# Kernel optimization log

Measured on AMD Instinct MI355X. Metric: run time of the kernel, lower is better.

Reference implementation:

```python
import jax, jax.numpy as jnp
import numpy as np

EPS = 1e-5

def _ln(x, g, b):
    m = x.mean(-1, keepdims=True)
    v = x.var(-1, keepdims=True)
    return (x - m) / jnp.sqrt(v + EPS) * g + b

def _dwconv(x, w, b, stride, pad):
    # x: [B,C,H,W], w: [C,1,k,k] depthwise
    C = x.shape[1]
    y = jax.lax.conv_general_dilated(
        x, w, (stride, stride), pad,
        feature_group_count=C,
        dimension_numbers=('NCHW', 'OIHW', 'NCHW'))
    return y + b[None, :, None, None]

def setup_inputs() -> dict:
    key = jax.random.key(0)
    ks = jax.random.split(key, 16)
    B, H, W, C = 8, 64, 64, 256
    N = H * W
    sr = 8
    d = {}
    d['x'] = jax.random.normal(ks[0], (B, N, C), jnp.float32)
    d['q_w'] = jax.random.normal(ks[1], (C, C), jnp.float32) * 0.02
    d['kv1_w'] = jax.random.normal(ks[2], (C, C), jnp.float32) * 0.02
    d['kv2_w'] = jax.random.normal(ks[3], (C, C), jnp.float32) * 0.02
    d['proj_w'] = jax.random.normal(ks[4], (C, C), jnp.float32) * 0.02
    d['proj_b'] = jnp.zeros((C,), jnp.float32)
    k1 = sr // 2
    d['sr1_w'] = jax.random.normal(ks[5], (C, 1, k1, k1), jnp.float32) * np.sqrt(2.0 / (k1 * k1))
    d['sr1_b'] = jnp.zeros((C,), jnp.float32)
    d['sr2_w'] = jax.random.normal(ks[6], (C, 1, sr, sr), jnp.float32) * np.sqrt(2.0 / (sr * sr))
    d['sr2_b'] = jnp.zeros((C,), jnp.float32)
    d['ln1_g'] = jnp.ones((C,), jnp.float32)
    d['ln1_b'] = jnp.zeros((C,), jnp.float32)
    d['ln2_g'] = jnp.ones((C,), jnp.float32)
    d['ln2_b'] = jnp.zeros((C,), jnp.float32)
    d['lc1_w'] = jax.random.normal(ks[7], (C // 2, 1, 3, 3), jnp.float32) * np.sqrt(2.0 / 9.0)
    d['lc1_b'] = jnp.zeros((C // 2,), jnp.float32)
    d['lc2_w'] = jax.random.normal(ks[8], (C // 2, 1, 3, 3), jnp.float32) * np.sqrt(2.0 / 9.0)
    d['lc2_b'] = jnp.zeros((C // 2,), jnp.float32)
    d['H'] = H
    d['W'] = W
    return d

def reference(x, q_w, kv1_w, kv2_w, proj_w, proj_b,
              sr1_w, sr1_b, sr2_w, sr2_b,
              ln1_g, ln1_b, ln2_g, ln2_b,
              lc1_w, lc1_b, lc2_w, lc2_b, H, W):
    B, N, C = x.shape
    nh = 8
    nh2 = nh // 2
    hd = C // nh
    sr = 8
    scale = hd ** -0.5

    # q: [B, nh, N, hd]
    q = jnp.einsum('bnc,dc->bnd', x, q_w).reshape(B, N, nh, hd).transpose(0, 2, 1, 3)

    x_ = x.transpose(0, 2, 1).reshape(B, C, H, W)
    x1 = _dwconv(x_, sr1_w, sr1_b, sr // 2, 'VALID')            # [B,C,H/4,W/4]
    x1 = x1.reshape(B, C, -1).transpose(0, 2, 1)                 # [B,N1,C]
    x1 = jax.nn.gelu(_ln(x1, ln1_g, ln1_b), approximate=False)
    x2 = _dwconv(x_, sr2_w, sr2_b, sr, 'VALID')                  # [B,C,H/8,W/8]
    x2 = x2.reshape(B, C, -1).transpose(0, 2, 1)                 # [B,N2,C]
    x2 = jax.nn.gelu(_ln(x2, ln2_g, ln2_b), approximate=False)

    def branch(xr, kv_w, qh, Hs, Ws, lc_w, lc_b):
        Bn, Ns, _ = xr.shape
        kv = jnp.einsum('bnc,dc->bnd', xr, kv_w).reshape(Bn, Ns, 2, nh2, hd).transpose(2, 0, 3, 1, 4)
        k, v = kv[0], kv[1]                                      # [B,nh2,Ns,hd]
        attn = jax.nn.softmax(jnp.einsum('bhqd,bhkd->bhqk', qh, k) * scale, axis=-1)
        # depthwise local conv injected into v
        v_sp = v.transpose(0, 2, 1, 3).reshape(Bn, Ns, C // 2).transpose(0, 2, 1).reshape(Bn, C // 2, Hs, Ws)
        v_lc = _dwconv(v_sp, lc_w, lc_b, 1, ((1, 1), (1, 1)))
        v = v + v_lc.reshape(Bn, nh2, hd, Ns).transpose(0, 1, 3, 2)
        out = jnp.einsum('bhqk,bhkd->bhqd', attn, v)             # [B,nh2,N,hd]
        return out.transpose(0, 2, 1, 3).reshape(Bn, N, C // 2)

    o1 = branch(x1, kv1_w, q[:, :nh2], H * 2 // sr, W * 2 // sr, lc1_w, lc1_b)
    o2 = branch(x2, kv2_w, q[:, nh2:], H // sr, W // sr, lc2_w, lc2_b)
    out = jnp.concatenate([o1, o2], axis=-1)
    return jnp.einsum('bnc,dc->bnd', out, proj_w) + proj_b
```

## Files before the change

### kernel.cpp

```cpp
#include <hip/hip_runtime.h>
#include <math.h>

static constexpr int Bb  = 8;
static constexpr int Nn  = 4096;
static constexpr int Cc  = 256;
static constexpr int Wd  = 64;
static constexpr int N1c = 256;
static constexpr int N2c = 64;

typedef __attribute__((ext_vector_type(8))) _Float16 f16x8;
typedef __attribute__((ext_vector_type(4))) _Float16 f16x4;
typedef __attribute__((ext_vector_type(4))) float    f32x4v;

__global__ __launch_bounds__(256)
void cvt4f16(const float* __restrict__ w0, const float* __restrict__ w1,
             const float* __restrict__ w2, const float* __restrict__ w3,
             _Float16* __restrict__ wf) {
  const int wsel = blockIdx.y;
  const float* w = wsel == 0 ? w0 : wsel == 1 ? w1 : wsel == 2 ? w2 : w3;
  const int i = (blockIdx.x * 256 + threadIdx.x) * 4;
  float4 v = *(const float4*)(w + i);
  f16x4 o = {(_Float16)v.x, (_Float16)v.y, (_Float16)v.z, (_Float16)v.w};
  *(f16x4*)(wf + (size_t)wsel * 65536 + i) = o;
}

template<bool A_HALF, bool OUT_HALF, bool BIAS>
__global__ __launch_bounds__(256)
void gemm_lds(const void* __restrict__ Ain, const _Float16* __restrict__ Wf,
              const float* __restrict__ bias, void* __restrict__ Outv) {
  __shared__ _Float16 Asl[2][64][40];
  __shared__ _Float16 Bsl[2][256][40];
  const int tid = threadIdx.x, lane = tid & 63, wid = tid >> 6;
  const int qi = lane & 15, g = lane >> 4;
  const int m0 = blockIdx.x * 64;
  const int ar = tid >> 2, ak = (tid & 3) * 8;

  const float*    pa32 = (const float*)Ain    + (size_t)(m0 + ar) * 256 + ak;
  const _Float16* pa16 = (const _Float16*)Ain + (size_t)(m0 + ar) * 256 + ak;
  const _Float16* pw   = Wf + (size_t)tid * 256;

  f32x4v acc[4][4] = {};
  f16x8 rA; f16x8 rB[4];

#define LDREG(k0)                                                        \
  do {                                                                   \
    if (A_HALF) {                                                        \
      rA = *(const f16x8*)(pa16 + (k0));                                 \
    } else {                                                             \
      float4 t0 = *(const float4*)(pa32 + (k0));                         \
      float4 t1 = *(const float4*)(pa32 + (k0) + 4);                     \
      rA = (f16x8){(_Float16)t0.x, (_Float16)t0.y, (_Float16)t0.z,       \
                   (_Float16)t0.w, (_Float16)t1.x, (_Float16)t1.y,       \
                   (_Float16)t1.z, (_Float16)t1.w};                      \
    }                                                                    \
    _Pragma("unroll")                                                    \
    for (int i = 0; i < 4; ++i) rB[i] = *(const f16x8*)(pw + (k0) + i * 8); \
  } while (0)

#define DSWRITE(buf)                                                     \
  do {                                                                   \
    *(f16x8*)&Asl[buf][ar][ak] = rA;                                     \
    _Pragma("unroll")                                                    \
    for (int i = 0; i < 4; ++i) *(f16x8*)&Bsl[buf][tid][i * 8] = rB[i];  \
  } while (0)

  LDREG(0);
  DSWRITE(0);
  LDREG(32);
  __syncthreads();

#pragma unroll
  for (int ks = 0; ks < 8; ++ks) {
    const int cur = ks & 1;
    if (ks < 7) DSWRITE(cur ^ 1);
    if (ks < 6) LDREG((ks + 2) * 32);
    f16x8 af[4], bf[4];
#pragma unroll
    for (int mt = 0; mt < 4; ++mt)
      af[mt] = *(const f16x8*)&Asl[cur][mt * 16 + qi][g * 8];
#pragma unroll
    for (int nt = 0; nt < 4; ++nt)
      bf[nt] = *(const f16x8*)&Bsl[cur][wid * 64 + nt * 16 + qi][g * 8];
#pragma unroll
    for (int nt = 0; nt < 4; ++nt)
#pragma unroll
      for (int mt = 0; mt < 4; ++mt)
        acc[mt][nt] = __builtin_amdgcn_mfma_f32_16x16x32_f16(af[mt], bf[nt], acc[mt][nt], 0, 0, 0);
    __syncthreads();
  }
#undef LDREG
#undef DSWRITE

#pragma unroll
  for (int nt = 0; nt < 4; ++nt) {
    const int col = wid * 64 + nt * 16 + qi;
    const float bv = BIAS ? bias[col] : 0.f;
#pragma unroll
    for (int mt = 0; mt < 4; ++mt) {
#pragma unroll
      for (int r = 0; r < 4; ++r) {
        const int row = m0 + mt * 16 + g * 4 + r;
        if (OUT_HALF)
          ((_Float16*)Outv)[(size_t)row * 256 + col] = (_Float16)acc[mt][nt][r];
        else
          ((float*)Outv)[(size_t)row * 256 + col] = acc[mt][nt][r] + bv;
      }
    }
  }
}

template<int KS, int HO>
__global__ __launch_bounds__(256)
void down_ln_gelu(const float* __restrict__ x, const float* __restrict__ w,
                  const float* __restrict__ cb, const float* __restrict__ g,
                  const float* __restrict__ lb, float* __restrict__ xo) {
  const int b = blockIdx.y;
  const int n1 = blockIdx.x;
  const int i = n1 / HO, j = n1 % HO;
  const int c = threadIdx.x;
  const float* wc = w + c * KS * KS;
  const float* xb = x + ((size_t)b * Nn) * Cc + c;
  float acc = cb[c];
#pragma unroll
  for (int dy = 0; dy < KS; ++dy) {
#pragma unroll
    for (int dx = 0; dx < KS; ++dx) {
      int n = (i * KS + dy) * Wd + (j * KS + dx);
      acc = fmaf(wc[dy * KS + dx], xb[(size_t)n * Cc], acc);
    }
  }
  float s = acc, s2 = acc * acc;
#pragma unroll
  for (int off = 32; off; off >>= 1) {
    s  += __shfl_down(s, off);
    s2 += __shfl_down(s2, off);
  }
  __shared__ float rs[4], rq[4];
  if ((c & 63) == 0) { rs[c >> 6] = s; rq[c >> 6] = s2; }
  __syncthreads();
  float sum = rs[0] + rs[1] + rs[2] + rs[3];
  float sq  = rq[0] + rq[1] + rq[2] + rq[3];
  float mean = sum * (1.f / Cc);
  float var  = sq * (1.f / Cc) - mean * mean;
  float xn = (acc - mean) * rsqrtf(var + 1e-5f) * g[c] + lb[c];
  float gel = 0.5f * xn * (1.f + erff(xn * 0.70710678118654752440f));
  xo[((size_t)b * (HO * HO) + n1) * Cc + c] = gel;
}

template<int HS>
__global__ __launch_bounds__(128)
void vconv(const float* __restrict__ kv, const float* __restrict__ w,
           const float* __restrict__ bias, float* __restrict__ vo) {
  constexpr int NS = HS * HS;
  const int b = blockIdx.y;
  const int n1 = blockIdx.x;
  const int i = n1 / HS, j = n1 % HS;
  const int c = threadIdx.x;
  const float* vb = kv + ((size_t)b * NS) * Cc + 128 + c;
  const float* wc = w + c * 9;
  float acc = bias[c];
#pragma unroll
  for (int dy = 0; dy < 3; ++dy) {
    int ii = i + dy - 1;
    if (ii < 0 || ii >= HS) continue;
#pragma unroll
    for (int dx = 0; dx < 3; ++dx) {
      int jj = j + dx - 1;
      if (jj < 0 || jj >= HS) continue;
      acc = fmaf(wc[dy * 3 + dx], vb[(size_t)(ii * HS + jj) * Cc], acc);
    }
  }
  vo[((size_t)b * NS + n1) * 128 + c] = acc + vb[(size_t)n1 * Cc];
}

template<int NS>
__global__ __launch_bounds__(256, 2)
void attn_f16(_Float16* __restrict__ qo, const float* __restrict__ kv,
              const float* __restrict__ vnew, const int branch) {
  constexpr int NT = NS / 16, NC = NS / 32, PS = NS + 8;
  constexpr float KC = 0.17677669529663688f * 1.4426950408889634f;
  __shared__ _Float16 Klds[NS][40];
  __shared__ _Float16 Vt[32][PS];
  __shared__ _Float16 Pl[64][PS];

  const int tid = threadIdx.x, lane = tid & 63, wid = tid >> 6;
  const int g = lane >> 4, qi = lane & 15;
  const int h = blockIdx.y, b = blockIdx.z;
  const int ck = h * 32;
  const int cq = branch * 128 + h * 32;

  for (int r = tid; r < NS; r += 256) {
    const float* kp = kv   + ((size_t)(b * NS + r)) * 256 + ck;
    const float* vp = vnew + ((size_t)(b * NS + r)) * 128 + ck;
    float kf[32], vf[32];
#pragma unroll
    for (int i = 0; i < 8; ++i) {
      *(float4*)&kf[i * 4] = *(const float4*)(kp + i * 4);
      *(float4*)&vf[i * 4] = *(const float4*)(vp + i * 4);
    }
#pragma unroll
    for (int i = 0; i < 4; ++i) {
      f16x8 kw;
#pragma unroll
      for (int j = 0; j < 8; ++j) kw[j] = (_Float16)kf[8 * i + j];
      *(f16x8*)&Klds[r][8 * i] = kw;
    }
#pragma unroll
    for (int d = 0; d < 32; ++d) Vt[d][r] = (_Float16)vf[d];
  }
  __syncthreads();

  f16x8 vt[2][NC];
#pragma unroll
  for (int dt = 0; dt < 2; ++dt)
#pragma unroll
    for (int c = 0; c < NC; ++c)
      vt[dt][c] = *(const f16x8*)&Vt[16 * dt + qi][32 * c + 8 * g];

  _Float16* Pw = &Pl[wid * 16 + qi][0];

  for (int qt = 0; qt < 4; ++qt) {
    const int qrow = blockIdx.x * 256 + wid * 64 + qt * 16 + qi;
    _Float16* qp = qo + ((size_t)b * Nn + qrow) * 256 + cq;
    f16x8 qfrag = *(const f16x8*)(qp + 8 * g);
    f32x4v s[NT];
#pragma unroll
    for (int t = 0; t < NT; ++t) {
      f16x8 kf = *(const f16x8*)&Klds[16 * t + qi][8 * g];
      s[t] = __builtin_amdgcn_mfma_f32_16x16x32_f16(kf, qfrag,
                                                    (f32x4v){0.f, 0.f, 0.f, 0.f}, 0, 0, 0);
    }
    float m = s[0][0];
#pragma unroll
    for (int t = 0; t < NT; ++t)
      m = fmaxf(m, fmaxf(fmaxf(s[t][0], s[t][1]), fmaxf(s[t][2], s[t][3])));
    m = fmaxf(m, __shfl_xor(m, 16));
    m = fmaxf(m, __shfl_xor(m, 32));
    float l = 0.f;
#pragma unroll
    for (int t = 0; t < NT; ++t)
#pragma unroll
      for (int r = 0; r < 4; ++r) {
        float p = exp2f((s[t][r] - m) * KC);
        s[t][r] = p; l += p;
      }
    l += __shfl_xor(l, 16);
    l += __shfl_xor(l, 32);
#pragma unroll
    for (int t = 0; t < NT; ++t) {
      f16x4 pw = {(_Float16)s[t][0], (_Float16)s[t][1],
                  (_Float16)s[t][2], (_Float16)s[t][3]};
      *(f16x4*)&Pw[16 * t + 4 * g] = pw;
    }
    f32x4v o0 = {0.f, 0.f, 0.f, 0.f}, o1 = {0.f, 0.f, 0.f, 0.f};
#pragma unroll
    for (int c = 0; c < NC; ++c) {
      f16x8 pf = *(const f16x8*)&Pw[32 * c + 8 * g];
      o0 = __builtin_amdgcn_mfma_f32_16x16x32_f16(vt[0][c], pf, o0, 0, 0, 0);
      o1 = __builtin_amdgcn_mfma_f32_16x16x32_f16(vt[1][c], pf, o1, 0, 0, 0);
    }
    const float inv = 1.f / l;
    f16x4 O0 = {(_Float16)(o0[0] * inv), (_Float16)(o0[1] * inv),
                (_Float16)(o0[2] * inv), (_Float16)(o0[3] * inv)};
    f16x4 O1 = {(_Float16)(o1[0] * inv), (_Float16)(o1[1] * inv),
                (_Float16)(o1[2] * inv), (_Float16)(o1[3] * inv)};
    *(f16x4*)(qp + 4 * g)      = O0;
    *(f16x4*)(qp + 16 + 4 * g) = O1;
  }
}

extern "C" void kernel_launch(void* const* d_in, const int* in_sizes, int n_in,
                              void* d_out, int out_size, void* d_ws, size_t ws_size,
                              hipStream_t stream) {
  const float* x      = (const float*)d_in[0];
  const float* q_w    = (const float*)d_in[1];
  const float* kv1_w  = (const float*)d_in[2];
  const float* kv2_w  = (const float*)d_in[3];
  const float* proj_w = (const float*)d_in[4];
  const float* proj_b = (const float*)d_in[5];
  const float* sr1_w  = (const float*)d_in[6];
  const float* sr1_b  = (const float*)d_in[7];
  const float* sr2_w  = (const float*)d_in[8];
  const float* sr2_b  = (const float*)d_in[9];
  const float* ln1_g  = (const float*)d_in[10];
  const float* ln1_b  = (const float*)d_in[11];
  const float* ln2_g  = (const float*)d_in[12];
  const float* ln2_b  = (const float*)d_in[13];
  const float* lc1_w  = (const float*)d_in[14];
  const float* lc1_b  = (const float*)d_in[15];
  const float* lc2_w  = (const float*)d_in[16];
  const float* lc2_b  = (const float*)d_in[17];
  float* out = (float*)d_out;
  float* ws  = (float*)d_ws;

  float* x1  = ws;
  float* kv1 = x1  + (size_t)Bb * N1c * Cc;
  float* vn1 = kv1 + (size_t)Bb * N1c * Cc;
  float* x2  = vn1 + (size_t)Bb * N1c * (Cc / 2);
  float* kv2 = x2  + (size_t)Bb * N2c * Cc;
  float* vn2 = kv2 + (size_t)Bb * N2c * Cc;
  float* fend = vn2 + (size_t)Bb * N2c * (Cc / 2);
  _Float16* wf = (_Float16*)fend;
  _Float16* qh = wf + (size_t)4 * 65536;

  cvt4f16<<<dim3(64, 4), 256, 0, stream>>>(q_w, kv1_w, kv2_w, proj_w, wf);
  gemm_lds<false, true, false><<<512, 256, 0, stream>>>(x, wf, nullptr, qh);
  down_ln_gelu<4, 16><<<dim3(N1c, Bb), 256, 0, stream>>>(x, sr1_w, sr1_b, ln1_g, ln1_b, x1);
  down_ln_gelu<8, 8><<<dim3(N2c, Bb), 256, 0, stream>>>(x, sr2_w, sr2_b, ln2_g, ln2_b, x2);
  gemm_lds<false, false, false><<<32, 256, 0, stream>>>(x1, wf + 65536,     nullptr, kv1);
  gemm_lds<false, false, false><<<8,  256, 0, stream>>>(x2, wf + 2 * 65536, nullptr, kv2);
  vconv<16><<<dim3(N1c, Bb), 128, 0, stream>>>(kv1, lc1_w, lc1_b, vn1);
  vconv<8> <<<dim3(N2c, Bb), 128, 0, stream>>>(kv2, lc2_w, lc2_b, vn2);
  attn_f16<256><<<dim3(16, 4, Bb), 256, 0, stream>>>(qh, kv1, vn1, 0);
  attn_f16<64> <<<dim3(16, 4, Bb), 256, 0, stream>>>(qh, kv2, vn2, 1);
  gemm_lds<true, false, true><<<512, 256, 0, stream>>>(qh, wf + 3 * 65536, proj_b, out);
}
```

Before: 109.9 us.

## Fuse both downsample branches into one pass and keep intermediates in fp16

Both depthwise downsample convolutions are now computed in one kernel that reads each 8x8 input patch once and produces the 4x4-strided outputs from the same registers. The conv weights are transposed up front for coalesced loads. The two kv GEMMs and the two value convolutions are each merged into a single launch. Intermediates (x1, x2, kv, v) are stored as fp16, which removes conversion work and halves their traffic, at some cost in precision for the small tensors.

```diff
diff --git a/kernel.cpp b/kernel.cpp
--- a/kernel.cpp
+++ b/kernel.cpp
@@ -4,7 +4,6 @@
 static constexpr int Bb  = 8;
 static constexpr int Nn  = 4096;
 static constexpr int Cc  = 256;
-static constexpr int Wd  = 64;
 static constexpr int N1c = 256;
 static constexpr int N2c = 64;
 
@@ -13,26 +12,33 @@
 typedef __attribute__((ext_vector_type(4))) float    f32x4v;
 
 __global__ __launch_bounds__(256)
-void cvt4f16(const float* __restrict__ w0, const float* __restrict__ w1,
-             const float* __restrict__ w2, const float* __restrict__ w3,
-             _Float16* __restrict__ wf) {
-  const int wsel = blockIdx.y;
-  const float* w = wsel == 0 ? w0 : wsel == 1 ? w1 : wsel == 2 ? w2 : w3;
-  const int i = (blockIdx.x * 256 + threadIdx.x) * 4;
-  float4 v = *(const float4*)(w + i);
-  f16x4 o = {(_Float16)v.x, (_Float16)v.y, (_Float16)v.z, (_Float16)v.w};
-  *(f16x4*)(wf + (size_t)wsel * 65536 + i) = o;
+void prep(const float* __restrict__ w0, const float* __restrict__ w1,
+          const float* __restrict__ w2, const float* __restrict__ w3,
+          const float* __restrict__ sr1w, const float* __restrict__ sr2w,
+          _Float16* __restrict__ wf, float* __restrict__ wt1, float* __restrict__ wt2) {
+  const int bid = blockIdx.x, c = threadIdx.x;
+  if (bid < 256) {
+    const int wsel = bid >> 6;
+    const float* w = wsel == 0 ? w0 : wsel == 1 ? w1 : wsel == 2 ? w2 : w3;
+    const int i = ((bid & 63) * 256 + c) * 4;
+    float4 v = *(const float4*)(w + i);
+    f16x4 o = {(_Float16)v.x, (_Float16)v.y, (_Float16)v.z, (_Float16)v.w};
+    *(f16x4*)(wf + (size_t)wsel * 65536 + i) = o;
+  } else {
+    const int row = bid - 256;
+    if (row < 16) wt1[row * 256 + c] = sr1w[c * 16 + row];
+    else { const int q = row - 16; wt2[q * 256 + c] = sr2w[c * 64 + q]; }
+  }
 }
 
 template<bool A_HALF, bool OUT_HALF, bool BIAS>
-__global__ __launch_bounds__(256)
-void gemm_lds(const void* __restrict__ Ain, const _Float16* __restrict__ Wf,
-              const float* __restrict__ bias, void* __restrict__ Outv) {
+__device__ __forceinline__
+void gemm_body(const void* __restrict__ Ain, const _Float16* __restrict__ Wf,
+               const float* __restrict__ bias, void* __restrict__ Outv, int m0) {
   __shared__ _Float16 Asl[2][64][40];
   __shared__ _Float16 Bsl[2][256][40];
   const int tid = threadIdx.x, lane = tid & 63, wid = tid >> 6;
   const int qi = lane & 15, g = lane >> 4;
-  const int m0 = blockIdx.x * 64;
   const int ar = tid >> 2, ak = (tid & 3) * 8;
 
   const float*    pa32 = (const float*)Ain    + (size_t)(m0 + ar) * 256 + ak;
@@ -109,74 +115,133 @@
   }
 }
 
-template<int KS, int HO>
+template<bool A_HALF, bool OUT_HALF, bool BIAS>
 __global__ __launch_bounds__(256)
-void down_ln_gelu(const float* __restrict__ x, const float* __restrict__ w,
-                  const float* __restrict__ cb, const float* __restrict__ g,
-                  const float* __restrict__ lb, float* __restrict__ xo) {
+void gemm_lds(const void* __restrict__ Ain, const _Float16* __restrict__ Wf,
+              const float* __restrict__ bias, void* __restrict__ Outv) {
+  gemm_body<A_HALF, OUT_HALF, BIAS>(Ain, Wf, bias, Outv, blockIdx.x * 64);
+}
+
+__global__ __launch_bounds__(256)
+void gemm_kv(const _Float16* __restrict__ A1, const _Float16* __restrict__ A2,
+             const _Float16* __restrict__ W1, const _Float16* __restrict__ W2,
+             _Float16* __restrict__ O1, _Float16* __restrict__ O2) {
+  const int bx = blockIdx.x;
+  if (bx < 32) gemm_body<true, true, false>(A1, W1, nullptr, O1, bx * 64);
+  else         gemm_body<true, true, false>(A2, W2, nullptr, O2, (bx - 32) * 64);
+}
+
+__global__ __launch_bounds__(256)
+void down2_ln_gelu(const float* __restrict__ x,
+                   const float* __restrict__ wt1, const float* __restrict__ b1,
+                   const float* __restrict__ g1, const float* __restrict__ lb1,
+                   const float* __restrict__ wt2, const float* __restrict__ b2,
+                   const float* __restrict__ g2, const float* __restrict__ lb2,
+                   _Float16* __restrict__ x1o, _Float16* __restrict__ x2o) {
   const int b = blockIdx.y;
-  const int n1 = blockIdx.x;
-  const int i = n1 / HO, j = n1 % HO;
+  const int n2 = blockIdx.x;
+  const int i2 = n2 >> 3, j2 = n2 & 7;
   const int c = threadIdx.x;
-  const float* wc = w + c * KS * KS;
+  const int lane = c & 63, wave = c >> 6;
   const float* xb = x + ((size_t)b * Nn) * Cc + c;
-  float acc = cb[c];
-#pragma unroll
-  for (int dy = 0; dy < KS; ++dy) {
-#pragma unroll
-    for (int dx = 0; dx < KS; ++dx) {
-      int n = (i * KS + dy) * Wd + (j * KS + dx);
-      acc = fmaf(wc[dy * KS + dx], xb[(size_t)n * Cc], acc);
-    }
-  }
-  float s = acc, s2 = acc * acc;
-#pragma unroll
-  for (int off = 32; off; off >>= 1) {
-    s  += __shfl_down(s, off);
-    s2 += __shfl_down(s2, off);
-  }
-  __shared__ float rs[4], rq[4];
-  if ((c & 63) == 0) { rs[c >> 6] = s; rq[c >> 6] = s2; }
+
+  float w1r[16];
+#pragma unroll
+  for (int t = 0; t < 16; ++t) w1r[t] = wt1[t * 256 + c];
+
+  float a2 = b2[c];
+  float a1[2][2] = {{b1[c], b1[c]}, {b1[c], b1[c]}};
+#pragma unroll
+  for (int dy = 0; dy < 8; ++dy) {
+    float vr[8], w2r[8];
+#pragma unroll
+    for (int dx = 0; dx < 8; ++dx) {
+      vr[dx]  = xb[(size_t)((8 * i2 + dy) * 64 + 8 * j2 + dx) * 256];
+      w2r[dx] = wt2[(dy * 8 + dx) * 256 + c];
+    }
+#pragma unroll
+    for (int dx = 0; dx < 8; ++dx) {
+      a2 = fmaf(w2r[dx], vr[dx], a2);
+      a1[dy >> 2][dx >> 2] = fmaf(w1r[(dy & 3) * 4 + (dx & 3)], vr[dx],
+                                  a1[dy >> 2][dx >> 2]);
+    }
+  }
+
+  float vals[5] = {a2, a1[0][0], a1[0][1], a1[1][0], a1[1][1]};
+  __shared__ float redS[4][5], redQ[4][5];
+  float sum[5], sq[5];
+#pragma unroll
+  for (int p = 0; p < 5; ++p) {
+    float s = vals[p], q2 = vals[p] * vals[p];
+#pragma unroll
+    for (int off = 1; off < 64; off <<= 1) {
+      s  += __shfl_xor(s, off);
+      q2 += __shfl_xor(q2, off);
+    }
+    if (lane == 0) { redS[wave][p] = s; redQ[wave][p] = q2; }
+  }
   __syncthreads();
-  float sum = rs[0] + rs[1] + rs[2] + rs[3];
-  float sq  = rq[0] + rq[1] + rq[2] + rq[3];
-  float mean = sum * (1.f / Cc);
-  float var  = sq * (1.f / Cc) - mean * mean;
-  float xn = (acc - mean) * rsqrtf(var + 1e-5f) * g[c] + lb[c];
-  float gel = 0.5f * xn * (1.f + erff(xn * 0.70710678118654752440f));
-  xo[((size_t)b * (HO * HO) + n1) * Cc + c] = gel;
+#pragma unroll
+  for (int p = 0; p < 5; ++p) {
+    sum[p] = redS[0][p] + redS[1][p] + redS[2][p] + redS[3][p];
+    sq[p]  = redQ[0][p] + redQ[1][p] + redQ[2][p] + redQ[3][p];
+  }
+#pragma unroll
+  for (int p = 0; p < 5; ++p) {
+    const float mean = sum[p] * (1.f / Cc);
+    const float var  = sq[p] * (1.f / Cc) - mean * mean;
+    const float gg = (p == 0) ? g2[c] : g1[c];
+    const float bb = (p == 0) ? lb2[c] : lb1[c];
+    const float xn = (vals[p] - mean) * rsqrtf(var + 1e-5f) * gg + bb;
+    const float gel = 0.5f * xn * (1.f + erff(xn * 0.70710678118654752440f));
+    if (p == 0) {
+      x2o[((size_t)b * N2c + n2) * 256 + c] = (_Float16)gel;
+    } else {
+      const int a = (p - 1) >> 1, bbx = (p - 1) & 1;
+      const int n1 = (2 * i2 + a) * 16 + (2 * j2 + bbx);
+      x1o[((size_t)b * N1c + n1) * 256 + c] = (_Float16)gel;
+    }
+  }
 }
 
 template<int HS>
-__global__ __launch_bounds__(128)
-void vconv(const float* __restrict__ kv, const float* __restrict__ w,
-           const float* __restrict__ bias, float* __restrict__ vo) {
+__device__ __forceinline__
+void vconv_body(const _Float16* __restrict__ kv, const float* __restrict__ w,
+                const float* __restrict__ bias, _Float16* __restrict__ vo,
+                int b, int n1, int c) {
   constexpr int NS = HS * HS;
-  const int b = blockIdx.y;
-  const int n1 = blockIdx.x;
   const int i = n1 / HS, j = n1 % HS;
-  const int c = threadIdx.x;
-  const float* vb = kv + ((size_t)b * NS) * Cc + 128 + c;
+  const _Float16* vb = kv + ((size_t)b * NS) * 256 + 128 + c;
   const float* wc = w + c * 9;
   float acc = bias[c];
 #pragma unroll
   for (int dy = 0; dy < 3; ++dy) {
-    int ii = i + dy - 1;
+    const int ii = i + dy - 1;
     if (ii < 0 || ii >= HS) continue;
 #pragma unroll
     for (int dx = 0; dx < 3; ++dx) {
-      int jj = j + dx - 1;
+      const int jj = j + dx - 1;
       if (jj < 0 || jj >= HS) continue;
-      acc = fmaf(wc[dy * 3 + dx], vb[(size_t)(ii * HS + jj) * Cc], acc);
-    }
-  }
-  vo[((size_t)b * NS + n1) * 128 + c] = acc + vb[(size_t)n1 * Cc];
+      acc = fmaf(wc[dy * 3 + dx], (float)vb[(size_t)(ii * HS + jj) * 256], acc);
+    }
+  }
+  vo[((size_t)b * NS + n1) * 128 + c] = (_Float16)(acc + (float)vb[(size_t)n1 * 256]);
+}
+
+__global__ __launch_bounds__(128)
+void vconv2(const _Float16* __restrict__ kv1, const _Float16* __restrict__ kv2,
+            const float* __restrict__ w1, const float* __restrict__ b1,
+            const float* __restrict__ w2, const float* __restrict__ b2,
+            _Float16* __restrict__ vn1, _Float16* __restrict__ vn2) {
+  const int bid = blockIdx.x, c = threadIdx.x;
+  if (bid < 2048) vconv_body<16>(kv1, w1, b1, vn1, bid >> 8, bid & 255, c);
+  else { const int t = bid - 2048; vconv_body<8>(kv2, w2, b2, vn2, t >> 6, t & 63, c); }
 }
 
 template<int NS>
 __global__ __launch_bounds__(256, 2)
-void attn_f16(_Float16* __restrict__ qo, const float* __restrict__ kv,
-              const float* __restrict__ vnew, const int branch) {
+void attn_f16(_Float16* __restrict__ qo, const _Float16* __restrict__ kv,
+              const _Float16* __restrict__ vnew, const int branch) {
   constexpr int NT = NS / 16, NC = NS / 32, PS = NS + 8;
   constexpr float KC = 0.17677669529663688f * 1.4426950408889634f;
   __shared__ _Float16 Klds[NS][40];
@@ -190,23 +255,17 @@
   const int cq = branch * 128 + h * 32;
 
   for (int r = tid; r < NS; r += 256) {
-    const float* kp = kv   + ((size_t)(b * NS + r)) * 256 + ck;
-    const float* vp = vnew + ((size_t)(b * NS + r)) * 128 + ck;
-    float kf[32], vf[32];
-#pragma unroll
-    for (int i = 0; i < 8; ++i) {
-      *(float4*)&kf[i * 4] = *(const float4*)(kp + i * 4);
-      *(float4*)&vf[i * 4] = *(const float4*)(vp + i * 4);
-    }
-#pragma unroll
-    for (int i = 0; i < 4; ++i) {
-      f16x8 kw;
-#pragma unroll
-      for (int j = 0; j < 8; ++j) kw[j] = (_Float16)kf[8 * i + j];
-      *(f16x8*)&Klds[r][8 * i] = kw;
-    }
-#pragma unroll
-    for (int d = 0; d < 32; ++d) Vt[d][r] = (_Float16)vf[d];
+    const _Float16* kp = kv   + ((size_t)(b * NS + r)) * 256 + ck;
+    const _Float16* vp = vnew + ((size_t)(b * NS + r)) * 128 + ck;
+#pragma unroll
+    for (int i = 0; i < 4; ++i)
+      *(f16x8*)&Klds[r][8 * i] = *(const f16x8*)(kp + 8 * i);
+    _Float16 va[32];
+#pragma unroll
+    for (int i = 0; i < 4; ++i)
+      *(f16x8*)&va[8 * i] = *(const f16x8*)(vp + 8 * i);
+#pragma unroll
+    for (int d = 0; d < 32; ++d) Vt[d][r] = va[d];
   }
   __syncthreads();
 
@@ -291,27 +350,26 @@
   const float* lc2_w  = (const float*)d_in[16];
   const float* lc2_b  = (const float*)d_in[17];
   float* out = (float*)d_out;
-  float* ws  = (float*)d_ws;
-
-  float* x1  = ws;
-  float* kv1 = x1  + (size_t)Bb * N1c * Cc;
-  float* vn1 = kv1 + (size_t)Bb * N1c * Cc;
-  float* x2  = vn1 + (size_t)Bb * N1c * (Cc / 2);
-  float* kv2 = x2  + (size_t)Bb * N2c * Cc;
-  float* vn2 = kv2 + (size_t)Bb * N2c * Cc;
-  float* fend = vn2 + (size_t)Bb * N2c * (Cc / 2);
-  _Float16* wf = (_Float16*)fend;
-  _Float16* qh = wf + (size_t)4 * 65536;
-
-  cvt4f16<<<dim3(64, 4), 256, 0, stream>>>(q_w, kv1_w, kv2_w, proj_w, wf);
+
+  char* wsb = (char*)d_ws;
+  _Float16* wf   = (_Float16*)wsb;
+  _Float16* qh   = wf + (size_t)4 * 65536;
+  _Float16* x1h  = qh + (size_t)Bb * Nn * Cc;
+  _Float16* x2h  = x1h + (size_t)Bb * N1c * Cc;
+  _Float16* kv1h = x2h + (size_t)Bb * N2c * Cc;
+  _Float16* kv2h = kv1h + (size_t)Bb * N1c * Cc;
+  _Float16* vn1h = kv2h + (size_t)Bb * N2c * Cc;
+  _Float16* vn2h = vn1h + (size_t)Bb * N1c * 128;
+  float* wt1 = (float*)(vn2h + (size_t)Bb * N2c * 128);
+  float* wt2 = wt1 + 16 * 256;
+
+  prep<<<336, 256, 0, stream>>>(q_w, kv1_w, kv2_w, proj_w, sr1_w, sr2_w, wf, wt1, wt2);
   gemm_lds<false, true, false><<<512, 256, 0, stream>>>(x, wf, nullptr, qh);
-  down_ln_gelu<4, 16><<<dim3(N1c, Bb), 256, 0, stream>>>(x, sr1_w, sr1_b, ln1_g, ln1_b, x1);
-  down_ln_gelu<8, 8><<<dim3(N2c, Bb), 256, 0, stream>>>(x, sr2_w, sr2_b, ln2_g, ln2_b, x2);
-  gemm_lds<false, false, false><<<32, 256, 0, stream>>>(x1, wf + 65536,     nullptr, kv1);
-  gemm_lds<false, false, false><<<8,  256, 0, stream>>>(x2, wf + 2 * 65536, nullptr, kv2);
-  vconv<16><<<dim3(N1c, Bb), 128, 0, stream>>>(kv1, lc1_w, lc1_b, vn1);
-  vconv<8> <<<dim3(N2c, Bb), 128, 0, stream>>>(kv2, lc2_w, lc2_b, vn2);
-  attn_f16<256><<<dim3(16, 4, Bb), 256, 0, stream>>>(qh, kv1, vn1, 0);
-  attn_f16<64> <<<dim3(16, 4, Bb), 256, 0, stream>>>(qh, kv2, vn2, 1);
+  down2_ln_gelu<<<dim3(64, Bb), 256, 0, stream>>>(x, wt1, sr1_b, ln1_g, ln1_b,
+                                                  wt2, sr2_b, ln2_g, ln2_b, x1h, x2h);
+  gemm_kv<<<40, 256, 0, stream>>>(x1h, x2h, wf + 65536, wf + 2 * 65536, kv1h, kv2h);
+  vconv2<<<2560, 128, 0, stream>>>(kv1h, kv2h, lc1_w, lc1_b, lc2_w, lc2_b, vn1h, vn2h);
+  attn_f16<256><<<dim3(16, 4, Bb), 256, 0, stream>>>(qh, kv1h, vn1h, 0);
+  attn_f16<64> <<<dim3(16, 4, Bb), 256, 0, stream>>>(qh, kv2h, vn2h, 1);
   gemm_lds<true, false, true><<<512, 256, 0, stream>>>(qh, wf + 3 * 65536, proj_b, out);
 }
```

Result: faster. 89.52 us (-18.5%).
